# Kernel optimization log

Measured on AMD Instinct MI355X. Metric: run time of the kernel, lower is better.

## Reference

```python
import jax, jax.numpy as jnp
import numpy as np

B, N, L = 32, 256, 50
DU, DI, DC = 32, 32, 16          # user / item / cate embed dims
D = DI + DC                       # item_feat_size = 48
N_USERS, N_ITEMS, N_CATES = 10001, 100000, 1001


def _linear_init(key, fan_in, fan_out):
    k1, k2 = jax.random.split(key)
    lim = 1.0 / np.sqrt(fan_in)
    w = jax.random.uniform(k1, (fan_in, fan_out), jnp.float32, -lim, lim)
    b = jax.random.uniform(k2, (fan_out,), jnp.float32, -lim, lim)
    return w, b


def setup_inputs() -> dict:
    key = jax.random.key(0)
    ks = jax.random.split(key, 16)

    def emb(k, n, d):
        # xavier-ish init, padding row 0 zeroed (padding_idx=0)
        t = jax.random.normal(k, (n, d), jnp.float32) * 0.02
        return t.at[0].set(0.0)

    emb_user = emb(ks[0], N_USERS, DU)
    emb_item = emb(ks[1], N_ITEMS, DI)
    emb_cate = emb(ks[2], N_CATES, DC)

    att_w1, att_b1 = _linear_init(ks[3], 4 * D, 64)   # LAU fc1 layer 1
    att_w2, att_b2 = _linear_init(ks[4], 64, 16)      # LAU fc1 layer 2
    att_w3, att_b3 = _linear_init(ks[5], 16, 1)       # LAU fc2

    TOT = DU + 2 * DI + 2 * DC                        # 128
    fc_w1, fc_b1 = _linear_init(ks[6], TOT, 200)
    fc_w2, fc_b2 = _linear_init(ks[7], 200, 80)
    fc_w3, fc_b3 = _linear_init(ks[8], 80, 1)

    user = jax.random.randint(ks[9], (B, N), 0, N_USERS)
    items = jax.random.randint(ks[10], (B, N), 0, N_ITEMS)
    items_cate = jax.random.randint(ks[11], (B, N), 0, N_CATES)
    interest_items = jax.random.randint(ks[12], (B, N, L), 0, N_ITEMS)
    interest_items_cate = jax.random.randint(ks[13], (B, N, L), 0, N_CATES)

    return dict(emb_user=emb_user, emb_item=emb_item, emb_cate=emb_cate,
                att_w1=att_w1, att_b1=att_b1, att_w2=att_w2, att_b2=att_b2,
                att_w3=att_w3, att_b3=att_b3,
                fc_w1=fc_w1, fc_b1=fc_b1, fc_w2=fc_w2, fc_b2=fc_b2,
                fc_w3=fc_w3, fc_b3=fc_b3,
                user=user, items=items, items_cate=items_cate,
                interest_items=interest_items,
                interest_items_cate=interest_items_cate)


def reference(emb_user, emb_item, emb_cate,
              att_w1, att_b1, att_w2, att_b2, att_w3, att_b3,
              fc_w1, fc_b1, fc_w2, fc_b2, fc_w3, fc_b3,
              user, items, items_cate, interest_items, interest_items_cate):
    u = emb_user[user]                                                 # [B,N,DU]
    ie = jnp.concatenate([emb_item[items], emb_cate[items_cate]], -1)  # [B,N,D]
    he = jnp.concatenate([emb_item[interest_items],
                          emb_cate[interest_items_cate]], -1)          # [B,N,L,D]

    # DIN local activation unit: cat(q, k, q-k, q*k) -> MLP -> scalar score
    q = jnp.broadcast_to(ie[:, :, None, :], he.shape)                  # [B,N,L,D]
    ai = jnp.concatenate([q, he, q - he, q * he], -1)                  # [B,N,L,4D]
    h = jax.nn.relu(ai @ att_w1 + att_b1)                              # [B,N,L,64]
    h = h @ att_w2 + att_b2                                            # [B,N,L,16]
    score = (h @ att_w3 + att_b3)[..., 0]                              # [B,N,L]

    # masked_fill(mask, 0) where mask = (interest_items == 0)
    score = jnp.where(interest_items == 0, 0.0, score)
    pooled = jnp.einsum('bnl,bnld->bnd', score, he)                    # [B,N,D]

    feat = jnp.concatenate([ie, pooled, u], -1)                        # [B,N,128]
    x = jax.nn.relu(feat @ fc_w1 + fc_b1)
    x = jax.nn.relu(x @ fc_w2 + fc_b2)
    logits = jax.nn.sigmoid((x @ fc_w3 + fc_b3)[..., 0])               # [B,N]

    logits = jnp.where(items == 0, -jnp.inf, logits)
    return jax.nn.softmax(logits, axis=-1)
```

## Files before the change

kernel.cpp:

```cpp
#include <hip/hip_runtime.h>
#include <math.h>


typedef short short8 __attribute__((ext_vector_type(8)));
typedef float f32x4 __attribute__((ext_vector_type(4)));

#define NL 50
#define BN_TOT 8192

__device__ __forceinline__ ushort f2bf(float x) {
    union { float f; uint u; } v; v.f = x;
    uint r = v.u + 0x7FFFu + ((v.u >> 16) & 1u);
    return (ushort)(r >> 16);
}
__device__ __forceinline__ float bf2f(ushort h) {
    union { uint u; float f; } v; v.u = ((uint)h) << 16;
    return v.f;
}

#define WS_FEAT   0
#define WS_LOGITS 2097152
#define WS_W1FRAG 2129920
#define WS_W2FRAG 2183168
#define WS_WCFRAG 2226176
#define WS_W1AC   2238464
#define WS_W23    2250752
#define WS_C23    2251008

__global__ __launch_bounds__(256) void k0_prep(
    const float* __restrict__ aw1, const float* __restrict__ ab2,
    const float* __restrict__ aw2, const float* __restrict__ aw3,
    const float* __restrict__ ab3,
    const float* __restrict__ fw1, const float* __restrict__ fw2,
    ushort* __restrict__ W1frag, ushort* __restrict__ W2frag,
    ushort* __restrict__ WcFrag, float* __restrict__ W1ac,
    float* __restrict__ w23, float* __restrict__ c23)
{
    const int b = blockIdx.x, t = threadIdx.x;
    if (b < 104) {
        int e = b * 256 + t;
        if (e < 26624) {
            int f = e >> 9, r = e & 511, l = r >> 3, j = r & 7;
            int nt = f >> 2, ks = f & 3;
            int k = ks * 32 + (l >> 4) * 8 + j, n = nt * 16 + (l & 15);
            float v = (n < 200) ? fw1[k * 200 + n] : 0.f;
            W1frag[e] = f2bf(v);
        }
    } else if (b < 188) {
        int e = (b - 104) * 256 + t;
        if (e < 21504) {
            int f = e >> 9, r = e & 511, l = r >> 3, j = r & 7;
            int nt = f / 7, ks = f % 7;
            int k = ks * 32 + (l >> 4) * 8 + j, n = nt * 16 + (l & 15);
            float v = (k < 200 && n < 80) ? fw2[k * 80 + n] : 0.f;
            W2frag[e] = f2bf(v);
        }
    } else if (b < 212) {
        int e = (b - 188) * 256 + t;
        int f = e >> 9, r = e & 511, l = r >> 3, j = r & 7;
        int nt = f / 3, ks = f % 3;
        int k = ks * 32 + (l >> 4) * 8 + j, n = nt * 16 + (l & 15);
        float v = (k < 48) ? (aw1[(48 + k) * 64 + n] - aw1[(96 + k) * 64 + n])
                           : aw1[(144 + (k - 48)) * 64 + n];
        WcFrag[e] = f2bf(v);
    } else if (b < 224) {
        int e = (b - 212) * 256 + t;
        if (e < 3072) {
            int k = e >> 6, j = e & 63;
            W1ac[e] = aw1[k * 64 + j] + aw1[(96 + k) * 64 + j];
        }
    } else {
        if (t < 64) {
            float s = 0.f;
            #pragma unroll
            for (int jj = 0; jj < 16; ++jj) s = fmaf(aw2[t * 16 + jj], aw3[jj], s);
            w23[t] = s;
        }
        if (t == 64) {
            float c = ab3[0];
            #pragma unroll
            for (int jj = 0; jj < 16; ++jj) c = fmaf(ab2[jj], aw3[jj], c);
            c23[0] = c;
        }
    }
}

__device__ __forceinline__ short8 lds8(const ushort* hb, int row, int c) {
    return *(const short8*)&hb[row * 56 + c * 8];
}
__device__ __forceinline__ short8 scale8(const ushort* hb, const float* qv,
                                         int row, int c, int qb) {
    short8 a = lds8(hb, row, c);
    union { short8 v; ushort s[8]; } o;
    const ushort* as = (const ushort*)&a;
    #pragma unroll
    for (int j = 0; j < 8; ++j) o.s[j] = f2bf(bf2f(as[j]) * qv[qb + j]);
    return o.v;
}

__global__ __launch_bounds__(256) void kA_attn(
    const float* __restrict__ emb_user,
    const float* __restrict__ emb_item,
    const float* __restrict__ emb_cate,
    const float* __restrict__ ab1,
    const int* __restrict__ user,
    const int* __restrict__ items,
    const int* __restrict__ cates,
    const int* __restrict__ ii,
    const int* __restrict__ ic,
    const ushort* __restrict__ WcFrag,
    const float* __restrict__ W1ac,
    const float* __restrict__ w23g,
    const float* __restrict__ c23g,
    ushort* __restrict__ feat)
{
    __shared__ __align__(16) ushort heb[4][64 * 56];
    __shared__ __align__(16) float  q_lds[4][48];
    __shared__ __align__(16) float  u_lds[4][32];
    __shared__ float  qc_lds[4][64];
    __shared__ float  sc_lds[4][52];
    __shared__ int    imll[4][52];
    __shared__ int    icll[4][52];

    const int t = threadIdx.x;
    const int w = t >> 6, l = t & 63;
    const int bn = blockIdx.x * 4 + w;
    const int col = l & 15, g = l >> 4;

    const int it = items[bn], ct = cates[bn], ur = user[bn];
    ushort* hb = &heb[w][0];
    float* qv = &q_lds[w][0];

    if (l < 12) {
        float4 v = (l < 8) ? ((const float4*)emb_item)[(size_t)it * 8 + l]
                           : ((const float4*)emb_cate)[(size_t)ct * 4 + (l - 8)];
        *(float4*)&q_lds[w][l * 4] = v;
    } else if (l >= 16 && l < 24) {
        *(float4*)&u_lds[w][(l - 16) * 4] = ((const float4*)emb_user)[(size_t)ur * 8 + (l - 16)];
    }
    if (l < NL) {
        imll[w][l] = ii[(size_t)bn * NL + l];
        icll[w][l] = ic[(size_t)bn * NL + l];
    }
    __syncthreads();

    #pragma unroll
    for (int e0 = 0; e0 < 384; e0 += 64) {
        int e = e0 + l;
        int row = e / 6, c = e - row * 6;
        union { short8 v; ushort s[8]; } o;
        o.v = short8{0,0,0,0,0,0,0,0};
        if (row < NL) {
            int k0 = c * 8;
            const float* src = (k0 < 32)
                ? emb_item + (size_t)imll[w][row] * 32 + k0
                : emb_cate + (size_t)icll[w][row] * 16 + (k0 - 32);
            float4 f0 = *(const float4*)src;
            float4 f1 = *(const float4*)(src + 4);
            o.s[0] = f2bf(f0.x); o.s[1] = f2bf(f0.y); o.s[2] = f2bf(f0.z); o.s[3] = f2bf(f0.w);
            o.s[4] = f2bf(f1.x); o.s[5] = f2bf(f1.y); o.s[6] = f2bf(f1.z); o.s[7] = f2bf(f1.w);
        }
        *(short8*)&hb[row * 56 + c * 8] = o.v;
    }

    {
        float a = ab1[l];
        #pragma unroll 8
        for (int k = 0; k < 48; ++k)
            a = fmaf(qv[k], W1ac[k * 64 + l], a);
        qc_lds[w][l] = a;
    }
    __syncthreads();

    f32x4 acc[4][4];
    #pragma unroll
    for (int m = 0; m < 4; ++m)
        #pragma unroll
        for (int n = 0; n < 4; ++n) acc[m][n] = f32x4{0,0,0,0};

    #pragma unroll
    for (int ks = 0; ks < 3; ++ks) {
        short8 af[4];
        #pragma unroll
        for (int mt = 0; mt < 4; ++mt) {
            int row = mt * 16 + col;
            if (ks == 0)       af[mt] = lds8(hb, row, g);
            else if (ks == 1)  af[mt] = (g < 2) ? lds8(hb, row, 4 + g)
                                                : scale8(hb, qv, row, g - 2, (g - 2) * 8);
            else               af[mt] = scale8(hb, qv, row, 2 + g, 16 + g * 8);
        }
        #pragma unroll
        for (int nt = 0; nt < 4; ++nt) {
            short8 bf = *(const short8*)&WcFrag[((nt * 3 + ks) * 64 + l) * 8];
            #pragma unroll
            for (int mt = 0; mt < 4; ++mt)
                acc[mt][nt] = __builtin_amdgcn_mfma_f32_16x16x32_bf16(af[mt], bf, acc[mt][nt], 0, 0, 0);
        }
    }

    {
        float qcv[4], wv[4];
        #pragma unroll
        for (int nt = 0; nt < 4; ++nt) {
            qcv[nt] = qc_lds[w][nt * 16 + col];
            wv[nt]  = w23g[nt * 16 + col];
        }
        float c23 = c23g[0];
        #pragma unroll
        for (int mt = 0; mt < 4; ++mt) {
            #pragma unroll
            for (int i = 0; i < 4; ++i) {
                float s = fmaxf(acc[mt][0][i] + qcv[0], 0.f) * wv[0]
                        + fmaxf(acc[mt][1][i] + qcv[1], 0.f) * wv[1]
                        + fmaxf(acc[mt][2][i] + qcv[2], 0.f) * wv[2]
                        + fmaxf(acc[mt][3][i] + qcv[3], 0.f) * wv[3];
                s += __shfl_xor(s, 1, 16);
                s += __shfl_xor(s, 2, 16);
                s += __shfl_xor(s, 4, 16);
                s += __shfl_xor(s, 8, 16);
                int row = mt * 16 + g * 4 + i;
                if (col == 0 && row < NL)
                    sc_lds[w][row] = (imll[w][row] == 0) ? 0.f : (s + c23);
            }
        }
    }
    __syncthreads();

    const size_t fb = (size_t)bn * 128;
    if (l < 48) {
        float p = 0.f;
        #pragma unroll 5
        for (int row = 0; row < NL; ++row)
            p = fmaf(sc_lds[w][row], bf2f(hb[row * 56 + l]), p);
        feat[fb + 48 + l] = f2bf(p);
        feat[fb + l] = f2bf(qv[l]);
    }
    if (l < 32) feat[fb + 96 + l] = f2bf(u_lds[w][l]);
}

__global__ __launch_bounds__(128) void k2_fc(
    const ushort* __restrict__ feat,
    const ushort* __restrict__ W1frag,
    const ushort* __restrict__ W2frag,
    const float* __restrict__ fb1, const float* __restrict__ fb2,
    const float* __restrict__ fw3, const float* __restrict__ fb3,
    const int* __restrict__ items,
    float* __restrict__ logits)
{
    __shared__ __align__(16) ushort x1s[2][16 * 256];

    const int t = threadIdx.x;
    const int wv = t >> 6, l = t & 63;
    const int r0 = blockIdx.x * 32 + wv * 16;
    const int col = l & 15, g = l >> 4;

    short8 afr[4];
    #pragma unroll
    for (int ks = 0; ks < 4; ++ks)
        afr[ks] = *(const short8*)&feat[(size_t)(r0 + col) * 128 + ks * 32 + g * 8];

    f32x4 acc[13];
    #pragma unroll
    for (int nt = 0; nt < 13; ++nt) acc[nt] = f32x4{0,0,0,0};
    #pragma unroll
    for (int nt = 0; nt < 13; ++nt)
        #pragma unroll
        for (int ks = 0; ks < 4; ++ks) {
            short8 bf = *(const short8*)&W1frag[((nt * 4 + ks) * 64 + l) * 8];
            acc[nt] = __builtin_amdgcn_mfma_f32_16x16x32_bf16(afr[ks], bf, acc[nt], 0, 0, 0);
        }

    if (l < 32) {
        int row = l >> 1, c = 26 + (l & 1);
        *(short8*)&x1s[wv][row * 256 + ((c ^ (row & 7)) << 3)] = short8{0,0,0,0,0,0,0,0};
    }
    #pragma unroll
    for (int nt = 0; nt < 13; ++nt) {
        int n = nt * 16 + col;
        float bias = (n < 200) ? fb1[n] : 0.f;
        #pragma unroll
        for (int i = 0; i < 4; ++i) {
            int row = g * 4 + i;
            float v = fmaxf(acc[nt][i] + bias, 0.f);
            int sw = (n >> 3) ^ (row & 7);
            x1s[wv][row * 256 + sw * 8 + (n & 7)] = f2bf(v);
        }
    }
    __syncthreads();

    f32x4 acc2[6];
    #pragma unroll
    for (int nt = 0; nt < 6; ++nt) acc2[nt] = f32x4{0,0,0,0};
    #pragma unroll
    for (int ks = 0; ks < 7; ++ks) {
        int chunk = ks * 4 + g;
        short8 a = *(const short8*)&x1s[wv][col * 256 + ((chunk ^ (col & 7)) << 3)];
        #pragma unroll
        for (int nt = 0; nt < 6; ++nt) {
            short8 bf = *(const short8*)&W2frag[((nt * 7 + ks) * 64 + l) * 8];
            acc2[nt] = __builtin_amdgcn_mfma_f32_16x16x32_bf16(a, bf, acc2[nt], 0, 0, 0);
        }
    }

    {
        float s[4] = {0.f, 0.f, 0.f, 0.f};
        #pragma unroll
        for (int nt = 0; nt < 5; ++nt) {
            int n = nt * 16 + col;
            float b2v = fb2[n], w3v = fw3[n];
            #pragma unroll
            for (int i = 0; i < 4; ++i)
                s[i] = fmaf(fmaxf(acc2[nt][i] + b2v, 0.f), w3v, s[i]);
        }
        #pragma unroll
        for (int i = 0; i < 4; ++i) {
            s[i] += __shfl_xor(s[i], 1, 16);
            s[i] += __shfl_xor(s[i], 2, 16);
            s[i] += __shfl_xor(s[i], 4, 16);
            s[i] += __shfl_xor(s[i], 8, 16);
        }
        if (col == 0) {
            float b3 = fb3[0];
            #pragma unroll
            for (int i = 0; i < 4; ++i) {
                int row = r0 + g * 4 + i;
                float lg = (items[row] == 0) ? -INFINITY
                                             : 1.f / (1.f + __expf(-(s[i] + b3)));
                logits[row] = lg;
            }
        }
    }
}

__global__ __launch_bounds__(256) void k3_softmax(
    const float* __restrict__ logits, float* __restrict__ out)
{
    const int b = blockIdx.x, t = threadIdx.x;
    __shared__ float red[4];
    float v = logits[b * 256 + t];
    float m = v;
    #pragma unroll
    for (int off = 32; off; off >>= 1) m = fmaxf(m, __shfl_xor(m, off, 64));
    if ((t & 63) == 0) red[t >> 6] = m;
    __syncthreads();
    float mx = fmaxf(fmaxf(red[0], red[1]), fmaxf(red[2], red[3]));
    float e = __expf(v - mx);
    float s = e;
    #pragma unroll
    for (int off = 32; off; off >>= 1) s += __shfl_xor(s, off, 64);
    __syncthreads();
    if ((t & 63) == 0) red[t >> 6] = s;
    __syncthreads();
    float tot = red[0] + red[1] + red[2] + red[3];
    out[b * 256 + t] = e / tot;
}

extern "C" void kernel_launch(void* const* d_in, const int* in_sizes, int n_in,
                              void* d_out, int out_size, void* d_ws, size_t ws_size,
                              hipStream_t stream)
{
    const float* emb_user = (const float*)d_in[0];
    const float* emb_item = (const float*)d_in[1];
    const float* emb_cate = (const float*)d_in[2];
    const float* aw1 = (const float*)d_in[3];
    const float* ab1 = (const float*)d_in[4];
    const float* aw2 = (const float*)d_in[5];
    const float* ab2 = (const float*)d_in[6];
    const float* aw3 = (const float*)d_in[7];
    const float* ab3 = (const float*)d_in[8];
    const float* fw1 = (const float*)d_in[9];
    const float* fb1 = (const float*)d_in[10];
    const float* fw2 = (const float*)d_in[11];
    const float* fb2 = (const float*)d_in[12];
    const float* fw3 = (const float*)d_in[13];
    const float* fb3 = (const float*)d_in[14];
    const int* user  = (const int*)d_in[15];
    const int* items = (const int*)d_in[16];
    const int* cates = (const int*)d_in[17];
    const int* ii    = (const int*)d_in[18];
    const int* ic    = (const int*)d_in[19];

    char* ws = (char*)d_ws;
    ushort* feat   = (ushort*)(ws + WS_FEAT);
    float*  logits = (float*) (ws + WS_LOGITS);
    ushort* W1frag = (ushort*)(ws + WS_W1FRAG);
    ushort* W2frag = (ushort*)(ws + WS_W2FRAG);
    ushort* WcFrag = (ushort*)(ws + WS_WCFRAG);
    float*  W1ac   = (float*) (ws + WS_W1AC);
    float*  w23    = (float*) (ws + WS_W23);
    float*  c23    = (float*) (ws + WS_C23);

    k0_prep<<<225, 256, 0, stream>>>(aw1, ab2, aw2, aw3, ab3, fw1, fw2,
                                     W1frag, W2frag, WcFrag, W1ac, w23, c23);
    kA_attn<<<BN_TOT / 4, 256, 0, stream>>>(emb_user, emb_item, emb_cate, ab1,
                                            user, items, cates, ii, ic,
                                            WcFrag, W1ac, w23, c23, feat);
    k2_fc<<<BN_TOT / 32, 128, 0, stream>>>(feat, W1frag, W2frag,
                                           fb1, fb2, fw3, fb3, items, logits);
    k3_softmax<<<32, 256, 0, stream>>>(logits, (float*)d_out);
}
```

Before: 152.1 us.

## Replace block barriers with wave-local LDS fences and use MFMA for query projection

Each wave in the attention and FC kernels owns its own LDS slice, so block-wide __syncthreads are replaced by a wave-local s_waitcnt lgkmcnt(0). The FC kernel becomes one wave per block. The per-item query projection (q·W1ac + bias) moves from a 48-step scalar FMA loop to a small bf16 MFMA, with the bias folded in through a constant-one column in a new prepacked fragment. Other edits skip the zero-padding rows in the gather, vectorise the pooling loop over scores, use the library bf16 conversion, and set launch bounds occupancy hints. The trade-off is that the query projection now runs in bf16 instead of fp32, and correctness depends on wave-private LDS access, with no cross-wave ordering.

```diff
diff --git a/kernel.cpp b/kernel.cpp
--- a/kernel.cpp
+++ b/kernel.cpp
@@ -1,4 +1,5 @@
 #include <hip/hip_runtime.h>
+#include <hip/hip_bf16.h>
 #include <math.h>
 
 
@@ -9,13 +10,16 @@
 #define BN_TOT 8192
 
 __device__ __forceinline__ ushort f2bf(float x) {
-    union { float f; uint u; } v; v.f = x;
-    uint r = v.u + 0x7FFFu + ((v.u >> 16) & 1u);
-    return (ushort)(r >> 16);
+    union { __hip_bfloat16 b; ushort u; } c;
+    c.b = __float2bfloat16(x);
+    return c.u;
 }
 __device__ __forceinline__ float bf2f(ushort h) {
     union { uint u; float f; } v; v.u = ((uint)h) << 16;
     return v.f;
+}
+__device__ __forceinline__ void wave_lds_fence() {
+    asm volatile("s_waitcnt lgkmcnt(0)" ::: "memory");
 }
 
 #define WS_FEAT   0
@@ -23,17 +27,18 @@
 #define WS_W1FRAG 2129920
 #define WS_W2FRAG 2183168
 #define WS_WCFRAG 2226176
-#define WS_W1AC   2238464
+#define WS_WACF   2238464
 #define WS_W23    2250752
 #define WS_C23    2251008
 
 __global__ __launch_bounds__(256) void k0_prep(
-    const float* __restrict__ aw1, const float* __restrict__ ab2,
+    const float* __restrict__ aw1, const float* __restrict__ ab1,
+    const float* __restrict__ ab2,
     const float* __restrict__ aw2, const float* __restrict__ aw3,
     const float* __restrict__ ab3,
     const float* __restrict__ fw1, const float* __restrict__ fw2,
     ushort* __restrict__ W1frag, ushort* __restrict__ W2frag,
-    ushort* __restrict__ WcFrag, float* __restrict__ W1ac,
+    ushort* __restrict__ WcFrag, ushort* __restrict__ WacF,
     float* __restrict__ w23, float* __restrict__ c23)
 {
     const int b = blockIdx.x, t = threadIdx.x;
@@ -63,12 +68,14 @@
         float v = (k < 48) ? (aw1[(48 + k) * 64 + n] - aw1[(96 + k) * 64 + n])
                            : aw1[(144 + (k - 48)) * 64 + n];
         WcFrag[e] = f2bf(v);
-    } else if (b < 224) {
+    } else if (b < 228) {
         int e = (b - 212) * 256 + t;
-        if (e < 3072) {
-            int k = e >> 6, j = e & 63;
-            W1ac[e] = aw1[k * 64 + j] + aw1[(96 + k) * 64 + j];
-        }
+        int f = e >> 9, r = e & 511, l = r >> 3, j = r & 7;
+        int nt = f >> 1, ks = f & 1;
+        int k = ks * 32 + (l >> 4) * 8 + j, n = nt * 16 + (l & 15);
+        float v = (k < 48) ? (aw1[k * 64 + n] + aw1[(96 + k) * 64 + n])
+                           : ((k == 48) ? ab1[n] : 0.f);
+        WacF[e] = f2bf(v);
     } else {
         if (t < 64) {
             float s = 0.f;
@@ -98,79 +105,105 @@
     return o.v;
 }
 
-__global__ __launch_bounds__(256) void kA_attn(
+__global__ __launch_bounds__(256, 4) void kA_attn(
     const float* __restrict__ emb_user,
     const float* __restrict__ emb_item,
     const float* __restrict__ emb_cate,
-    const float* __restrict__ ab1,
     const int* __restrict__ user,
     const int* __restrict__ items,
     const int* __restrict__ cates,
     const int* __restrict__ ii,
     const int* __restrict__ ic,
     const ushort* __restrict__ WcFrag,
-    const float* __restrict__ W1ac,
+    const ushort* __restrict__ WacF,
     const float* __restrict__ w23g,
     const float* __restrict__ c23g,
     ushort* __restrict__ feat)
 {
     __shared__ __align__(16) ushort heb[4][64 * 56];
-    __shared__ __align__(16) float  q_lds[4][48];
-    __shared__ __align__(16) float  u_lds[4][32];
-    __shared__ float  qc_lds[4][64];
-    __shared__ float  sc_lds[4][52];
-    __shared__ int    imll[4][52];
-    __shared__ int    icll[4][52];
+    __shared__ __align__(16) float  qf[4][48];
+    __shared__ __align__(16) float  uf[4][32];
+    __shared__ __align__(16) float  qcl[4][64];
+    __shared__ __align__(16) float  scl[4][52];
+    __shared__ int    iml[4][52];
+    __shared__ int    icl[4][52];
 
     const int t = threadIdx.x;
     const int w = t >> 6, l = t & 63;
     const int bn = blockIdx.x * 4 + w;
     const int col = l & 15, g = l >> 4;
 
-    const int it = items[bn], ct = cates[bn], ur = user[bn];
     ushort* hb = &heb[w][0];
-    float* qv = &q_lds[w][0];
+    const float* qv = &qf[w][0];
 
     if (l < 12) {
-        float4 v = (l < 8) ? ((const float4*)emb_item)[(size_t)it * 8 + l]
+        int it_ = items[bn], ct = cates[bn];
+        float4 v = (l < 8) ? ((const float4*)emb_item)[(size_t)it_ * 8 + l]
                            : ((const float4*)emb_cate)[(size_t)ct * 4 + (l - 8)];
-        *(float4*)&q_lds[w][l * 4] = v;
+        *(float4*)&qf[w][l * 4] = v;
     } else if (l >= 16 && l < 24) {
-        *(float4*)&u_lds[w][(l - 16) * 4] = ((const float4*)emb_user)[(size_t)ur * 8 + (l - 16)];
+        int ur = user[bn];
+        *(float4*)&uf[w][(l - 16) * 4] = ((const float4*)emb_user)[(size_t)ur * 8 + (l - 16)];
     }
     if (l < NL) {
-        imll[w][l] = ii[(size_t)bn * NL + l];
-        icll[w][l] = ic[(size_t)bn * NL + l];
-    }
-    __syncthreads();
-
-    #pragma unroll
-    for (int e0 = 0; e0 < 384; e0 += 64) {
+        iml[w][l] = ii[(size_t)bn * NL + l];
+        icl[w][l] = ic[(size_t)bn * NL + l];
+    }
+    wave_lds_fence();
+
+    #pragma unroll
+    for (int e0 = 0; e0 < 300; e0 += 64) {
         int e = e0 + l;
-        int row = e / 6, c = e - row * 6;
-        union { short8 v; ushort s[8]; } o;
-        o.v = short8{0,0,0,0,0,0,0,0};
-        if (row < NL) {
+        if (e < 300) {
+            int row = e / 6, c = e - row * 6;
             int k0 = c * 8;
             const float* src = (k0 < 32)
-                ? emb_item + (size_t)imll[w][row] * 32 + k0
-                : emb_cate + (size_t)icll[w][row] * 16 + (k0 - 32);
+                ? emb_item + (size_t)iml[w][row] * 32 + k0
+                : emb_cate + (size_t)icl[w][row] * 16 + (k0 - 32);
             float4 f0 = *(const float4*)src;
             float4 f1 = *(const float4*)(src + 4);
+            union { short8 v; ushort s[8]; } o;
             o.s[0] = f2bf(f0.x); o.s[1] = f2bf(f0.y); o.s[2] = f2bf(f0.z); o.s[3] = f2bf(f0.w);
             o.s[4] = f2bf(f1.x); o.s[5] = f2bf(f1.y); o.s[6] = f2bf(f1.z); o.s[7] = f2bf(f1.w);
-        }
-        *(short8*)&hb[row * 56 + c * 8] = o.v;
-    }
+            *(short8*)&hb[row * 56 + c * 8] = o.v;
+        }
+    }
+    wave_lds_fence();
 
     {
-        float a = ab1[l];
-        #pragma unroll 8
-        for (int k = 0; k < 48; ++k)
-            a = fmaf(qv[k], W1ac[k * 64 + l], a);
-        qc_lds[w][l] = a;
-    }
-    __syncthreads();
+        short8 afq[2];
+        #pragma unroll
+        for (int ks = 0; ks < 2; ++ks) {
+            union { short8 v; ushort s[8]; } a;
+            a.v = short8{0,0,0,0,0,0,0,0};
+            if (col == 0) {
+                int k0 = ks * 32 + g * 8;
+                if (k0 < 48) {
+                    float4 x = *(const float4*)&qf[w][k0];
+                    float4 y = *(const float4*)&qf[w][k0 + 4];
+                    a.s[0] = f2bf(x.x); a.s[1] = f2bf(x.y); a.s[2] = f2bf(x.z); a.s[3] = f2bf(x.w);
+                    a.s[4] = f2bf(y.x); a.s[5] = f2bf(y.y); a.s[6] = f2bf(y.z); a.s[7] = f2bf(y.w);
+                } else if (k0 == 48) {
+                    a.s[0] = 0x3F80;
+                }
+            }
+            afq[ks] = a.v;
+        }
+        f32x4 aq[4];
+        #pragma unroll
+        for (int nt = 0; nt < 4; ++nt) {
+            aq[nt] = f32x4{0,0,0,0};
+            #pragma unroll
+            for (int ks = 0; ks < 2; ++ks) {
+                short8 bq = *(const short8*)&WacF[((nt * 2 + ks) * 64 + l) * 8];
+                aq[nt] = __builtin_amdgcn_mfma_f32_16x16x32_bf16(afq[ks], bq, aq[nt], 0, 0, 0);
+            }
+        }
+        if (g == 0) {
+            #pragma unroll
+            for (int nt = 0; nt < 4; ++nt) qcl[w][nt * 16 + col] = aq[nt][0];
+        }
+    }
 
     f32x4 acc[4][4];
     #pragma unroll
@@ -197,12 +230,13 @@
                 acc[mt][nt] = __builtin_amdgcn_mfma_f32_16x16x32_bf16(af[mt], bf, acc[mt][nt], 0, 0, 0);
         }
     }
+    wave_lds_fence();
 
     {
         float qcv[4], wv[4];
         #pragma unroll
         for (int nt = 0; nt < 4; ++nt) {
-            qcv[nt] = qc_lds[w][nt * 16 + col];
+            qcv[nt] = qcl[w][nt * 16 + col];
             wv[nt]  = w23g[nt * 16 + col];
         }
         float c23 = c23g[0];
@@ -220,25 +254,33 @@
                 s += __shfl_xor(s, 8, 16);
                 int row = mt * 16 + g * 4 + i;
                 if (col == 0 && row < NL)
-                    sc_lds[w][row] = (imll[w][row] == 0) ? 0.f : (s + c23);
+                    scl[w][row] = (iml[w][row] == 0) ? 0.f : (s + c23);
             }
         }
     }
-    __syncthreads();
+    wave_lds_fence();
 
     const size_t fb = (size_t)bn * 128;
     if (l < 48) {
         float p = 0.f;
-        #pragma unroll 5
-        for (int row = 0; row < NL; ++row)
-            p = fmaf(sc_lds[w][row], bf2f(hb[row * 56 + l]), p);
+        #pragma unroll
+        for (int r4 = 0; r4 < 48; r4 += 4) {
+            float4 sv = *(const float4*)&scl[w][r4];
+            p = fmaf(sv.x, bf2f(hb[(r4 + 0) * 56 + l]), p);
+            p = fmaf(sv.y, bf2f(hb[(r4 + 1) * 56 + l]), p);
+            p = fmaf(sv.z, bf2f(hb[(r4 + 2) * 56 + l]), p);
+            p = fmaf(sv.w, bf2f(hb[(r4 + 3) * 56 + l]), p);
+        }
+        float2 st = *(const float2*)&scl[w][48];
+        p = fmaf(st.x, bf2f(hb[48 * 56 + l]), p);
+        p = fmaf(st.y, bf2f(hb[49 * 56 + l]), p);
         feat[fb + 48 + l] = f2bf(p);
         feat[fb + l] = f2bf(qv[l]);
     }
-    if (l < 32) feat[fb + 96 + l] = f2bf(u_lds[w][l]);
-}
-
-__global__ __launch_bounds__(128) void k2_fc(
+    if (l < 32) feat[fb + 96 + l] = f2bf(uf[w][l]);
+}
+
+__global__ __launch_bounds__(64, 4) void k2_fc(
     const ushort* __restrict__ feat,
     const ushort* __restrict__ W1frag,
     const ushort* __restrict__ W2frag,
@@ -247,11 +289,10 @@
     const int* __restrict__ items,
     float* __restrict__ logits)
 {
-    __shared__ __align__(16) ushort x1s[2][16 * 256];
-
-    const int t = threadIdx.x;
-    const int wv = t >> 6, l = t & 63;
-    const int r0 = blockIdx.x * 32 + wv * 16;
+    __shared__ __align__(16) ushort x1s[16 * 256];
+
+    const int l = threadIdx.x;
+    const int r0 = blockIdx.x * 16;
     const int col = l & 15, g = l >> 4;
 
     short8 afr[4];
@@ -272,7 +313,7 @@
 
     if (l < 32) {
         int row = l >> 1, c = 26 + (l & 1);
-        *(short8*)&x1s[wv][row * 256 + ((c ^ (row & 7)) << 3)] = short8{0,0,0,0,0,0,0,0};
+        *(short8*)&x1s[row * 256 + ((c ^ (row & 7)) << 3)] = short8{0,0,0,0,0,0,0,0};
     }
     #pragma unroll
     for (int nt = 0; nt < 13; ++nt) {
@@ -283,10 +324,10 @@
             int row = g * 4 + i;
             float v = fmaxf(acc[nt][i] + bias, 0.f);
             int sw = (n >> 3) ^ (row & 7);
-            x1s[wv][row * 256 + sw * 8 + (n & 7)] = f2bf(v);
-        }
-    }
-    __syncthreads();
+            x1s[row * 256 + sw * 8 + (n & 7)] = f2bf(v);
+        }
+    }
+    wave_lds_fence();
 
     f32x4 acc2[6];
     #pragma unroll
@@ -294,7 +335,7 @@
     #pragma unroll
     for (int ks = 0; ks < 7; ++ks) {
         int chunk = ks * 4 + g;
-        short8 a = *(const short8*)&x1s[wv][col * 256 + ((chunk ^ (col & 7)) << 3)];
+        short8 a = *(const short8*)&x1s[col * 256 + ((chunk ^ (col & 7)) << 3)];
         #pragma unroll
         for (int nt = 0; nt < 6; ++nt) {
             short8 bf = *(const short8*)&W2frag[((nt * 7 + ks) * 64 + l) * 8];
@@ -386,16 +427,16 @@
     ushort* W1frag = (ushort*)(ws + WS_W1FRAG);
     ushort* W2frag = (ushort*)(ws + WS_W2FRAG);
     ushort* WcFrag = (ushort*)(ws + WS_WCFRAG);
-    float*  W1ac   = (float*) (ws + WS_W1AC);
+    ushort* WacF   = (ushort*)(ws + WS_WACF);
     float*  w23    = (float*) (ws + WS_W23);
     float*  c23    = (float*) (ws + WS_C23);
 
-    k0_prep<<<225, 256, 0, stream>>>(aw1, ab2, aw2, aw3, ab3, fw1, fw2,
-                                     W1frag, W2frag, WcFrag, W1ac, w23, c23);
-    kA_attn<<<BN_TOT / 4, 256, 0, stream>>>(emb_user, emb_item, emb_cate, ab1,
+    k0_prep<<<229, 256, 0, stream>>>(aw1, ab1, ab2, aw2, aw3, ab3, fw1, fw2,
+                                     W1frag, W2frag, WcFrag, WacF, w23, c23);
+    kA_attn<<<BN_TOT / 4, 256, 0, stream>>>(emb_user, emb_item, emb_cate,
                                             user, items, cates, ii, ic,
-                                            WcFrag, W1ac, w23, c23, feat);
-    k2_fc<<<BN_TOT / 32, 128, 0, stream>>>(feat, W1frag, W2frag,
-                                           fb1, fb2, fw3, fb3, items, logits);
+                                            WcFrag, WacF, w23, c23, feat);
+    k2_fc<<<BN_TOT / 16, 64, 0, stream>>>(feat, W1frag, W2frag,
+                                          fb1, fb2, fw3, fb3, items, logits);
     k3_softmax<<<32, 256, 0, stream>>>(logits, (float*)d_out);
 }
```

After: 142.1 us. 1.07x faster.
